# Optimization experiments

Measured on AMD Instinct MI355X. Metric: run time of the kernel, lower is better.

## Reference

```python
import jax, jax.numpy as jnp
import numpy as np

N = 20000      # nodes
E = 320000     # edges
F = 32         # node_feat_dim
H = 128        # hidden_dim
HEADS = 4
DH = 128       # out_channels per head (PyG TransformerConv semantics)
L = 2          # number of GNNBlocks actually built


def _ln(x, s, b, eps=1e-5):
    m = x.mean(-1, keepdims=True)
    v = ((x - m) ** 2).mean(-1, keepdims=True)
    return (x - m) / jnp.sqrt(v + eps) * s + b


def setup_inputs() -> dict:
    key = jax.random.key(0)
    ks = jax.random.split(key, 16)
    nrm = lambda k, sh, sc=0.05: jax.random.normal(k, sh, dtype=jnp.float32) * sc
    inp = {}
    inp['x'] = jax.random.normal(ks[0], (N, F), dtype=jnp.float32)
    inp['edge_index'] = jax.random.randint(ks[1], (2, E), 0, N)
    inp['Win'] = nrm(ks[2], (F, H))
    inp['b_in'] = jnp.zeros((H,), jnp.float32)
    inp['ln1_s'] = jnp.ones((L, H), jnp.float32)
    inp['ln1_b'] = jnp.zeros((L, H), jnp.float32)
    inp['Wq'] = nrm(ks[3], (L, H, HEADS * DH))
    inp['bq'] = jnp.zeros((L, HEADS * DH), jnp.float32)
    inp['Wk'] = nrm(ks[4], (L, H, HEADS * DH))
    inp['bk'] = jnp.zeros((L, HEADS * DH), jnp.float32)
    inp['Wv'] = nrm(ks[5], (L, H, HEADS * DH))
    inp['bv'] = jnp.zeros((L, HEADS * DH), jnp.float32)
    inp['Wskip'] = nrm(ks[6], (L, H, H))
    inp['bskip'] = jnp.zeros((L, H), jnp.float32)
    inp['Wbeta'] = nrm(ks[7], (L, 3 * H, 1))
    inp['ln2_s'] = jnp.ones((L, H), jnp.float32)
    inp['ln2_b'] = jnp.zeros((L, H), jnp.float32)
    inp['W1'] = nrm(ks[8], (L, H, 4 * H))
    inp['b1'] = jnp.zeros((L, 4 * H), jnp.float32)
    inp['W2'] = nrm(ks[9], (L, 4 * H, H))
    inp['b2'] = jnp.zeros((L, H), jnp.float32)
    inp['g1'] = jnp.ones((L,), jnp.float32)
    inp['g2'] = jnp.ones((L,), jnp.float32)
    inp['lno_s'] = jnp.ones((H,), jnp.float32)
    inp['lno_b'] = jnp.zeros((H,), jnp.float32)
    return inp


def reference(x, edge_index, Win, b_in, ln1_s, ln1_b, Wq, bq, Wk, bk, Wv, bv,
              Wskip, bskip, Wbeta, ln2_s, ln2_b, W1, b1, W2, b2, g1, g2,
              lno_s, lno_b):
    src, dst = edge_index[0], edge_index[1]  # messages flow src -> dst
    n = x.shape[0]
    scale = 1.0 / np.sqrt(DH).astype(np.float32)
    h = x @ Win + b_in  # [N,H]
    for l in range(L):
        # --- pre-norm TransformerConv (heads=4, concat=False, beta=True) ---
        hn = _ln(h, ln1_s[l], ln1_b[l])
        q = (hn @ Wq[l] + bq[l]).reshape(n, HEADS, DH)
        k = (hn @ Wk[l] + bk[l]).reshape(n, HEADS, DH)
        v = (hn @ Wv[l] + bv[l]).reshape(n, HEADS, DH)
        # per-edge attention logits [E, HEADS]
        alpha = jnp.einsum('ehd,ehd->eh', q[dst], k[src]) * scale
        # segment softmax over incoming edges of each target node
        amax = jax.ops.segment_max(alpha, dst, num_segments=n)  # [N,HEADS]
        num = jnp.exp(alpha - amax[dst])
        den = jax.ops.segment_sum(num, dst, num_segments=n)      # [N,HEADS]
        a = num / den[dst]                                       # [E,HEADS]
        # scatter-aggregate weighted values, then mean over heads (concat=False)
        agg = jax.ops.segment_sum(a[:, :, None] * v[src], dst, num_segments=n)
        out = agg.mean(axis=1)                                   # [N,H]
        # root skip + beta gate
        xr = hn @ Wskip[l] + bskip[l]
        beta = jax.nn.sigmoid(
            jnp.concatenate([out, xr, out - xr], axis=-1) @ Wbeta[l])  # [N,1]
        attn = beta * xr + (1.0 - beta) * out
        h = h + g1[l] * attn
        # --- pre-norm FFN ---
        hn2 = _ln(h, ln2_s[l], ln2_b[l])
        ffn = jax.nn.gelu(hn2 @ W1[l] + b1[l], approximate=False) @ W2[l] + b2[l]
        h = h + g2[l] * ffn
    return _ln(h, lno_s, lno_b)
```

## Files before the change

### kernel.cpp

```cpp
#include <hip/hip_runtime.h>
#include <hip/hip_bf16.h>
#include <math.h>

#define NN 20000
#define NE 320000

typedef unsigned short ushort_t;
typedef unsigned short ushortx8 __attribute__((ext_vector_type(8)));
typedef short s16x8 __attribute__((ext_vector_type(8)));
typedef float f32x4 __attribute__((ext_vector_type(4)));
typedef float f32x2 __attribute__((ext_vector_type(2)));

__device__ __forceinline__ float us2f(unsigned short u){
  return __uint_as_float(((unsigned)u) << 16);
}
__device__ __forceinline__ unsigned short f2us(float f){
  unsigned u = __float_as_uint(f);
  unsigned r = (u + 0x7fffu + ((u >> 16) & 1u)) >> 16;
  return (unsigned short)r;
}
__device__ __forceinline__ void e4m3x8_to_f32(uint2 d, float* out){
  f32x2 a = __builtin_amdgcn_cvt_pk_f32_fp8(d.x, false);
  f32x2 b = __builtin_amdgcn_cvt_pk_f32_fp8(d.x, true);
  f32x2 c = __builtin_amdgcn_cvt_pk_f32_fp8(d.y, false);
  f32x2 e = __builtin_amdgcn_cvt_pk_f32_fp8(d.y, true);
  out[0] = a.x; out[1] = a.y; out[2] = b.x; out[3] = b.y;
  out[4] = c.x; out[5] = c.y; out[6] = e.x; out[7] = e.y;
}
__device__ __forceinline__ uint2 f32x8_to_e4m3(const float* f){
  unsigned lo = __builtin_amdgcn_cvt_pk_fp8_f32(f[0], f[1], 0u, false);
  lo = __builtin_amdgcn_cvt_pk_fp8_f32(f[2], f[3], lo, true);
  unsigned hi = __builtin_amdgcn_cvt_pk_fp8_f32(f[4], f[5], 0u, false);
  hi = __builtin_amdgcn_cvt_pk_fp8_f32(f[6], f[7], hi, true);
  return make_uint2(lo, hi);
}

__global__ void k_hist(const int* __restrict__ ei, int* __restrict__ deg){
  int e = blockIdx.x * 256 + threadIdx.x;
  if (e < NE) atomicAdd(&deg[ei[NE + e]], 1);
}

__global__ __launch_bounds__(1024) void k_scan(const int* __restrict__ deg,
                                               int* __restrict__ rowst,
                                               int* __restrict__ cur){
  __shared__ int s[1024];
  __shared__ int carry_s;
  int tid = threadIdx.x;
  if (tid == 0) carry_s = 0;
  __syncthreads();
  for (int base = 0; base < NN; base += 1024){
    int v = (base + tid < NN) ? deg[base + tid] : 0;
    s[tid] = v; __syncthreads();
    for (int off = 1; off < 1024; off <<= 1){
      int t = (tid >= off) ? s[tid - off] : 0;
      __syncthreads();
      s[tid] += t;
      __syncthreads();
    }
    int carry = carry_s;
    int excl = carry + s[tid] - v;
    if (base + tid < NN){ rowst[base + tid] = excl; cur[base + tid] = excl; }
    __syncthreads();
    if (tid == 0) carry_s = carry + s[1023];
    __syncthreads();
  }
  if (tid == 0) rowst[NN] = carry_s;
}

__global__ void k_scatter(const int* __restrict__ ei, int* __restrict__ cur,
                          int* __restrict__ srcs){
  int e = blockIdx.x * 256 + threadIdx.x;
  if (e < NE){
    int s = ei[e];
    int d = ei[NE + e];
    int p = atomicAdd(&cur[d], 1);
    srcs[p] = s;
  }
}

__global__ void k_wt(const float* __restrict__ Wq, const float* __restrict__ Wk,
                     const float* __restrict__ Wv, const float* __restrict__ Wsk,
                     const float* __restrict__ W1, const float* __restrict__ W2,
                     const float* __restrict__ bq, const float* __restrict__ bk,
                     const float* __restrict__ bv, const float* __restrict__ bsk,
                     ushort_t* __restrict__ out, float* __restrict__ bcat,
                     int* __restrict__ deg){
  int f = blockIdx.x * 256 + threadIdx.x;
  if (f < 688128){
    float val;
    if (f < 425984){
      int l = f / 212992, idx = f % 212992;
      int n = idx / 128, kk = idx % 128;
      if (n < 512)       val = Wq[(size_t)l * 65536 + kk * 512 + n];
      else if (n < 1024) val = Wk[(size_t)l * 65536 + kk * 512 + (n - 512)];
      else if (n < 1536) val = Wv[(size_t)l * 65536 + kk * 512 + (n - 1024)];
      else               val = Wsk[(size_t)l * 16384 + kk * 128 + (n - 1536)];
    } else if (f < 557056){
      int idx = f - 425984;
      int l = idx / 65536, r = idx % 65536;
      int n = r / 128, kk = r % 128;
      val = W1[(size_t)l * 65536 + kk * 512 + n];
    } else {
      int idx = f - 557056;
      int l = idx / 65536, r = idx % 65536;
      int n = r / 512, kk = r % 512;
      val = W2[(size_t)l * 65536 + kk * 128 + n];
    }
    out[f] = f2us(val);
  } else if (f < 691456){
    int i = f - 688128;
    int l = i / 1664, c = i % 1664;
    float v;
    if (c < 512)       v = bq[l * 512 + c];
    else if (c < 1024) v = bk[l * 512 + c - 512];
    else if (c < 1536) v = bv[l * 512 + c - 1024];
    else               v = bsk[l * 128 + c - 1536];
    bcat[i] = v;
  } else if (f < 711456){
    deg[f - 691456] = 0;
  }
}

__global__ __launch_bounds__(128) void k_inproj(const float* __restrict__ x,
                                                const float* __restrict__ Win,
                                                const float* __restrict__ bin,
                                                float* __restrict__ h){
  __shared__ float sW[32 * 128];
  __shared__ float sx[4][32];
  int tid = threadIdx.x;
  for (int i = 0; i < 32; i++) sW[i * 128 + tid] = Win[i * 128 + tid];
  int r0 = blockIdx.x * 4;
  {
    int r = tid >> 5, kk = tid & 31;
    int gr = r0 + r;
    sx[r][kk] = (gr < NN) ? x[gr * 32 + kk] : 0.f;
  }
  __syncthreads();
  float bias = bin[tid];
  for (int r = 0; r < 4; r++){
    int gr = r0 + r;
    if (gr >= NN) break;
    float acc = bias;
    #pragma unroll
    for (int k2 = 0; k2 < 32; k2++) acc += sx[r][k2] * sW[k2 * 128 + tid];
    h[(size_t)gr * 128 + tid] = acc;
  }
}

template<int OUTBF16>
__global__ void k_ln(const float* __restrict__ in, const float* __restrict__ sc,
                     const float* __restrict__ bi, void* __restrict__ outp, int rows){
  int row = blockIdx.x * 4 + (threadIdx.x >> 6);
  int lane = threadIdx.x & 63;
  if (row >= rows) return;
  const float* p = in + (size_t)row * 128 + lane * 2;
  float x0 = p[0], x1 = p[1];
  float sum = x0 + x1;
  for (int m = 1; m < 64; m <<= 1) sum += __shfl_xor(sum, m);
  float mean = sum * (1.f / 128.f);
  float d0 = x0 - mean, d1 = x1 - mean;
  float vs = d0 * d0 + d1 * d1;
  for (int m = 1; m < 64; m <<= 1) vs += __shfl_xor(vs, m);
  float rstd = rsqrtf(vs * (1.f / 128.f) + 1e-5f);
  int d = lane * 2;
  float o0 = d0 * rstd * sc[d] + bi[d];
  float o1 = d1 * rstd * sc[d + 1] + bi[d + 1];
  if (OUTBF16){
    ushort_t* o = (ushort_t*)outp + (size_t)row * 128 + d;
    o[0] = f2us(o0); o[1] = f2us(o1);
  } else {
    float* o = (float*)outp + (size_t)row * 128 + d;
    o[0] = o0; o[1] = o1;
  }
}

template<int MODE>
__global__ __launch_bounds__(256) void k_mm(const ushort_t* __restrict__ A, int M, int K,
                                            const ushort_t* __restrict__ Bt,
                                            const float* __restrict__ bias,
                                            void* __restrict__ Cp, int ldc,
                                            const float* __restrict__ gptr,
                                            ushort_t* __restrict__ qout,
                                            unsigned char* __restrict__ kvout,
                                            ushort_t* __restrict__ xrout){
  __shared__ ushort_t smem[2 * 128 * 72];
  ushort_t* As = smem;
  ushort_t* Bs = smem + 128 * 72;
  int tid = threadIdx.x;
  int m0 = blockIdx.x * 128, n0 = blockIdx.y * 128;
  int lane = tid & 63, w = tid >> 6;
  int wm = (w >> 1) * 64, wn = (w & 1) * 64;
  int fr = lane & 15, fq = lane >> 4;
  f32x4 acc[4][4];
  #pragma unroll
  for (int i = 0; i < 4; i++)
    #pragma unroll
    for (int j = 0; j < 4; j++) acc[i][j] = (f32x4){0.f, 0.f, 0.f, 0.f};

  for (int k0 = 0; k0 < K; k0 += 64){
    __syncthreads();
    #pragma unroll
    for (int it = 0; it < 4; it++){
      int idx = it * 256 + tid;
      int row = idx >> 3, ks = (idx & 7) * 8;
      int gr = m0 + row; if (gr >= M) gr = M - 1;
      *(ushortx8*)&As[row * 72 + ks] = *(const ushortx8*)(A + (size_t)gr * K + k0 + ks);
      *(ushortx8*)&Bs[row * 72 + ks] = *(const ushortx8*)(Bt + (size_t)(n0 + row) * K + k0 + ks);
    }
    __syncthreads();
    #pragma unroll
    for (int ks = 0; ks < 64; ks += 32){
      s16x8 a[4], b[4];
      #pragma unroll
      for (int i = 0; i < 4; i++)
        a[i] = *(const s16x8*)&As[(wm + i * 16 + fr) * 72 + ks + fq * 8];
      #pragma unroll
      for (int j = 0; j < 4; j++)
        b[j] = *(const s16x8*)&Bs[(wn + j * 16 + fr) * 72 + ks + fq * 8];
      #pragma unroll
      for (int i = 0; i < 4; i++)
        #pragma unroll
        for (int j = 0; j < 4; j++)
          acc[i][j] = __builtin_amdgcn_mfma_f32_16x16x32_bf16(a[i], b[j], acc[i][j], 0, 0, 0);
    }
  }

  if (MODE == 2){
    float g = *gptr;
    #pragma unroll
    for (int i = 0; i < 4; i++){
      int grb = m0 + wm + i * 16 + fq * 4;
      #pragma unroll
      for (int r = 0; r < 4; r++){
        int gr = grb + r;
        if (gr >= M) continue;
        #pragma unroll
        for (int j = 0; j < 4; j++){
          int gc = n0 + wn + j * 16 + fr;
          float c = acc[i][j][r] + bias[gc];
          ((float*)Cp)[(size_t)gr * ldc + gc] += g * c;
        }
      }
    }
    return;
  }

  __syncthreads();
  ushort_t* Cs = smem;
  #pragma unroll
  for (int i = 0; i < 4; i++){
    int rowb = wm + i * 16 + fq * 4;
    #pragma unroll
    for (int j = 0; j < 4; j++){
      int col = wn + j * 16 + fr;
      float bv = bias[n0 + col];
      #pragma unroll
      for (int r = 0; r < 4; r++){
        float c = acc[i][j][r] + bv;
        if (MODE == 1) c = 0.5f * c * (1.f + erff(c * 0.70710678118654752f));
        Cs[(rowb + r) * 136 + col] = f2us(c);
      }
    }
  }
  __syncthreads();
  #pragma unroll
  for (int it = 0; it < 8; it++){
    int idx = it * 256 + tid;
    int row = idx >> 4, seg = idx & 15;
    int gr = m0 + row;
    if (gr >= M) continue;
    ushortx8 cv = *(const ushortx8*)&Cs[row * 136 + seg * 8];
    int gc = n0 + seg * 8;
    if (MODE == 1){
      *(ushortx8*)((ushort_t*)Cp + (size_t)gr * ldc + gc) = cv;
    } else {
      if (n0 < 512){
        *(ushortx8*)(qout + (size_t)gr * 512 + gc) = cv;
      } else if (n0 < 1536){
        float fv[8];
        #pragma unroll
        for (int t = 0; t < 8; t++) fv[t] = us2f(cv[t]);
        *(uint2*)(kvout + (size_t)gr * 1024 + (gc - 512)) = f32x8_to_e4m3(fv);
      } else {
        *(ushortx8*)(xrout + (size_t)gr * 128 + (gc - 1536)) = cv;
      }
    }
  }
}

__global__ void k_alpha(const ushort_t* __restrict__ q, const unsigned char* __restrict__ kv8,
                        const int* __restrict__ rowst, const int* __restrict__ srcs,
                        float* __restrict__ alw){
  int n = blockIdx.x * 4 + (threadIdx.x >> 6);
  int lane = threadIdx.x & 63;
  if (n >= NN) return;
  int s0 = rowst[n], s1 = rowst[n + 1];
  if (s0 == s1) return;
  ushortx8 qv = *((const ushortx8*)(q + (size_t)n * 512) + lane);
  float qf[8];
  #pragma unroll
  for (int t = 0; t < 8; t++) qf[t] = us2f(qv[t]);
  const float scale = 0.08838834764831845f;
  int head = lane >> 4;
  for (int c0 = s0; c0 < s1; c0 += 64){
    int rem = s1 - c0; if (rem > 64) rem = 64;
    int se = (lane < rem) ? srcs[c0 + lane] : 0;
    int j = 0;
    for (; j + 4 <= rem; j += 4){
      int sv[4];
      #pragma unroll
      for (int u = 0; u < 4; u++) sv[u] = __shfl(se, j + u);
      uint2 kd[4];
      #pragma unroll
      for (int u = 0; u < 4; u++)
        kd[u] = *((const uint2*)(kv8 + (size_t)sv[u] * 1024) + lane);
      float p[4] = {0.f, 0.f, 0.f, 0.f};
      #pragma unroll
      for (int u = 0; u < 4; u++){
        float kf[8];
        e4m3x8_to_f32(kd[u], kf);
        #pragma unroll
        for (int t = 0; t < 8; t++) p[u] += qf[t] * kf[t];
      }
      #pragma unroll
      for (int u = 0; u < 4; u++){
        p[u] += __shfl_xor(p[u], 1); p[u] += __shfl_xor(p[u], 2);
        p[u] += __shfl_xor(p[u], 4); p[u] += __shfl_xor(p[u], 8);
      }
      if ((lane & 15) == 0){
        #pragma unroll
        for (int u = 0; u < 4; u++) alw[(size_t)(c0 + j + u) * 4 + head] = __expf(p[u] * scale);
      }
    }
    for (; j < rem; j++){
      int sv0 = __shfl(se, j);
      uint2 kd = *((const uint2*)(kv8 + (size_t)sv0 * 1024) + lane);
      float kf[8];
      e4m3x8_to_f32(kd, kf);
      float p0 = 0.f;
      #pragma unroll
      for (int t = 0; t < 8; t++) p0 += qf[t] * kf[t];
      p0 += __shfl_xor(p0, 1); p0 += __shfl_xor(p0, 2);
      p0 += __shfl_xor(p0, 4); p0 += __shfl_xor(p0, 8);
      if ((lane & 15) == 0) alw[(size_t)(c0 + j) * 4 + head] = __expf(p0 * scale);
    }
  }
}

__global__ void k_node(const float* __restrict__ alw, const unsigned char* __restrict__ kv8,
                       const int* __restrict__ rowst, const int* __restrict__ srcs,
                       const ushort_t* __restrict__ xr, const float* __restrict__ Wb,
                       const float* __restrict__ g1p, float* __restrict__ h,
                       const float* __restrict__ sc2, const float* __restrict__ bi2,
                       ushort_t* __restrict__ hn){
  int n = blockIdx.x * 4 + (threadIdx.x >> 6);
  int lane = threadIdx.x & 63;
  if (n >= NN) return;
  int s0 = rowst[n], s1 = rowst[n + 1];
  int deg = s1 - s0;
  int head = lane >> 4;
  float l = 0.f;
  float acc[8] = {0.f, 0.f, 0.f, 0.f, 0.f, 0.f, 0.f, 0.f};
  for (int c0 = s0; c0 < s1; c0 += 64){
    int rem = s1 - c0; if (rem > 64) rem = 64;
    int se = (lane < rem) ? srcs[c0 + lane] : 0;
    int j = 0;
    for (; j + 4 <= rem; j += 4){
      int sv[4];
      #pragma unroll
      for (int u = 0; u < 4; u++) sv[u] = __shfl(se, j + u);
      uint2 vd[4];
      #pragma unroll
      for (int u = 0; u < 4; u++)
        vd[u] = *((const uint2*)(kv8 + (size_t)sv[u] * 1024 + 512) + lane);
      float wv[4];
      #pragma unroll
      for (int u = 0; u < 4; u++) wv[u] = alw[(size_t)(c0 + j + u) * 4 + head];
      #pragma unroll
      for (int u = 0; u < 4; u++){
        float vf[8];
        e4m3x8_to_f32(vd[u], vf);
        l += wv[u];
        #pragma unroll
        for (int t = 0; t < 8; t++) acc[t] += wv[u] * vf[t];
      }
    }
    for (; j < rem; j++){
      int sv0 = __shfl(se, j);
      uint2 vd = *((const uint2*)(kv8 + (size_t)sv0 * 1024 + 512) + lane);
      float vf[8];
      e4m3x8_to_f32(vd, vf);
      float ww = alw[(size_t)(c0 + j) * 4 + head];
      l += ww;
      #pragma unroll
      for (int t = 0; t < 8; t++) acc[t] += ww * vf[t];
    }
  }
  float inv = deg ? (0.25f / l) : 0.f;
  #pragma unroll
  for (int t = 0; t < 8; t++){
    float r = acc[t] * inv;
    r += __shfl_xor(r, 16); r += __shfl_xor(r, 32);
    acc[t] = r;
  }
  if (lane < 16){
    int d = lane * 8;
    float xv[8];
    {
      ushortx8 xrv = *(const ushortx8*)(xr + (size_t)n * 128 + d);
      #pragma unroll
      for (int t = 0; t < 8; t++) xv[t] = us2f(xrv[t]);
    }
    float pp = 0.f;
    #pragma unroll
    for (int t = 0; t < 8; t++){
      float w0 = Wb[d + t], w1 = Wb[128 + d + t], w2 = Wb[256 + d + t];
      pp += acc[t] * (w0 + w2) + xv[t] * (w1 - w2);
    }
    pp += __shfl_xor(pp, 1); pp += __shfl_xor(pp, 2);
    pp += __shfl_xor(pp, 4); pp += __shfl_xor(pp, 8);
    float beta = 1.f / (1.f + __expf(-pp));
    float g = *g1p;
    float* hp = h + (size_t)n * 128 + d;
    float hv[8];
    {
      float4 h0 = *(const float4*)(hp);
      float4 h1 = *(const float4*)(hp + 4);
      hv[0]=h0.x; hv[1]=h0.y; hv[2]=h0.z; hv[3]=h0.w;
      hv[4]=h1.x; hv[5]=h1.y; hv[6]=h1.z; hv[7]=h1.w;
    }
    #pragma unroll
    for (int t = 0; t < 8; t++)
      hv[t] += g * (beta * xv[t] + (1.f - beta) * acc[t]);
    float s = 0.f;
    #pragma unroll
    for (int t = 0; t < 8; t++) s += hv[t];
    s += __shfl_xor(s, 1); s += __shfl_xor(s, 2);
    s += __shfl_xor(s, 4); s += __shfl_xor(s, 8);
    float mean = s * (1.f / 128.f);
    float vs = 0.f;
    #pragma unroll
    for (int t = 0; t < 8; t++){ float dd = hv[t] - mean; vs += dd * dd; }
    vs += __shfl_xor(vs, 1); vs += __shfl_xor(vs, 2);
    vs += __shfl_xor(vs, 4); vs += __shfl_xor(vs, 8);
    float rstd = rsqrtf(vs * (1.f / 128.f) + 1e-5f);
    *(float4*)(hp) = make_float4(hv[0], hv[1], hv[2], hv[3]);
    *(float4*)(hp + 4) = make_float4(hv[4], hv[5], hv[6], hv[7]);
    ushortx8 hno;
    #pragma unroll
    for (int t = 0; t < 8; t++)
      hno[t] = f2us((hv[t] - mean) * rstd * sc2[d + t] + bi2[d + t]);
    *(ushortx8*)(hn + (size_t)n * 128 + d) = hno;
  }
}

extern "C" void kernel_launch(void* const* d_in, const int* in_sizes, int n_in,
                              void* d_out, int out_size, void* d_ws, size_t ws_size,
                              hipStream_t stream){
  const float* x    = (const float*)d_in[0];
  const int*   ei   = (const int*)d_in[1];
  const float* Win  = (const float*)d_in[2];
  const float* bin  = (const float*)d_in[3];
  const float* ln1s = (const float*)d_in[4];
  const float* ln1b = (const float*)d_in[5];
  const float* Wq   = (const float*)d_in[6];
  const float* bq   = (const float*)d_in[7];
  const float* Wk   = (const float*)d_in[8];
  const float* bk   = (const float*)d_in[9];
  const float* Wv   = (const float*)d_in[10];
  const float* bv   = (const float*)d_in[11];
  const float* Wsk  = (const float*)d_in[12];
  const float* bsk  = (const float*)d_in[13];
  const float* Wbt  = (const float*)d_in[14];
  const float* ln2s = (const float*)d_in[15];
  const float* ln2b = (const float*)d_in[16];
  const float* W1   = (const float*)d_in[17];
  const float* b1   = (const float*)d_in[18];
  const float* W2   = (const float*)d_in[19];
  const float* b2   = (const float*)d_in[20];
  const float* g1   = (const float*)d_in[21];
  const float* g2   = (const float*)d_in[22];
  const float* lnos = (const float*)d_in[23];
  const float* lnob = (const float*)d_in[24];

  char* wsb = (char*)d_ws;
  size_t off = 0;
  float*         h    = (float*)(wsb + off);         off += (size_t)NN * 128 * 4;
  ushort_t*      hn   = (ushort_t*)(wsb + off);      off += (size_t)NN * 128 * 2;
  ushort_t*      qbuf = (ushort_t*)(wsb + off);      off += (size_t)NN * 512 * 2;
  unsigned char* kv8  = (unsigned char*)(wsb + off); off += (size_t)NN * 1024;
  ushort_t*      xrb  = (ushort_t*)(wsb + off);      off += (size_t)NN * 128 * 2;
  ushort_t*      tb   = (ushort_t*)(wsb + off);      off += (size_t)NN * 512 * 2;
  float*         alw  = (float*)(wsb + off);         off += (size_t)NE * 4 * 4;
  ushort_t*      wt   = (ushort_t*)(wsb + off);      off += (size_t)688128 * 2;
  float*         bcat = (float*)(wsb + off);         off += (size_t)3328 * 4;
  int*           deg   = (int*)(wsb + off);          off += (size_t)NN * 4;
  int*           rowst = (int*)(wsb + off);          off += (size_t)(NN + 4) * 4;
  int*           cur   = (int*)(wsb + off);          off += (size_t)NN * 4;
  int*           srcs  = (int*)(wsb + off);          off += (size_t)NE * 4;
  ushort_t* Wcat = wt;
  ushort_t* W1t  = wt + 425984;
  ushort_t* W2t  = wt + 557056;

  k_wt<<<2780, 256, 0, stream>>>(Wq, Wk, Wv, Wsk, W1, W2, bq, bk, bv, bsk, wt, bcat, deg);
  k_hist<<<(NE + 255) / 256, 256, 0, stream>>>(ei, deg);
  k_scan<<<1, 1024, 0, stream>>>(deg, rowst, cur);
  k_scatter<<<(NE + 255) / 256, 256, 0, stream>>>(ei, cur, srcs);
  k_inproj<<<(NN + 3) / 4, 128, 0, stream>>>(x, Win, bin, h);

  dim3 gQ(157, 13), gF1(157, 4), gF2(157, 1);
  for (int l = 0; l < 2; l++){
    k_ln<1><<<(NN + 3) / 4, 256, 0, stream>>>(h, ln1s + l * 128, ln1b + l * 128, hn, NN);
    k_mm<3><<<gQ, 256, 0, stream>>>(hn, NN, 128, Wcat + (size_t)l * 212992, bcat + l * 1664,
                                    nullptr, 0, nullptr, qbuf, kv8, xrb);
    k_alpha<<<(NN + 3) / 4, 256, 0, stream>>>(qbuf, kv8, rowst, srcs, alw);
    k_node<<<(NN + 3) / 4, 256, 0, stream>>>(alw, kv8, rowst, srcs, xrb, Wbt + l * 384,
                                             g1 + l, h, ln2s + l * 128, ln2b + l * 128, hn);
    k_mm<1><<<gF1, 256, 0, stream>>>(hn, NN, 128, W1t + (size_t)l * 65536, b1 + l * 512,
                                     tb, 512, nullptr, nullptr, nullptr, nullptr);
    k_mm<2><<<gF2, 256, 0, stream>>>(tb, NN, 512, W2t + (size_t)l * 65536, b2 + l * 128,
                                     h, 128, g2 + l, nullptr, nullptr, nullptr);
  }
  k_ln<0><<<(NN + 3) / 4, 256, 0, stream>>>(h, lnos, lnob, (float*)d_out, NN);
}
```

Before: 465.1 us.

## Fuse attention logits into aggregation with interleaved fp8 K/V layout

Merges the separate logit kernel into the node aggregation kernel, so exp(q·k) weights are computed on the fly and the per-edge weight buffer is no longer written and reread. K and V fp8 rows are interleaved per 8-element chunk so one 16-byte load per lane fetches both K and V for an edge. It also replaces the shared-memory scan with a wave-shuffle scan and makes the input projection process 16 rows per block. The cost is more work and registers per thread in the fused kernel, which may reduce occupancy.

```diff
diff --git a/kernel.cpp b/kernel.cpp
--- a/kernel.cpp
+++ b/kernel.cpp
@@ -43,28 +43,34 @@
 __global__ __launch_bounds__(1024) void k_scan(const int* __restrict__ deg,
                                                int* __restrict__ rowst,
                                                int* __restrict__ cur){
-  __shared__ int s[1024];
-  __shared__ int carry_s;
+  __shared__ int ws[16];
   int tid = threadIdx.x;
-  if (tid == 0) carry_s = 0;
-  __syncthreads();
+  int lane = tid & 63, wid = tid >> 6;
+  int carry = 0;
   for (int base = 0; base < NN; base += 1024){
-    int v = (base + tid < NN) ? deg[base + tid] : 0;
-    s[tid] = v; __syncthreads();
-    for (int off = 1; off < 1024; off <<= 1){
-      int t = (tid >= off) ? s[tid - off] : 0;
-      __syncthreads();
-      s[tid] += t;
-      __syncthreads();
-    }
-    int carry = carry_s;
-    int excl = carry + s[tid] - v;
-    if (base + tid < NN){ rowst[base + tid] = excl; cur[base + tid] = excl; }
+    int i = base + tid;
+    int v = (i < NN) ? deg[i] : 0;
+    int incl = v;
+    #pragma unroll
+    for (int off = 1; off < 64; off <<= 1){
+      int t = __shfl_up(incl, off);
+      if (lane >= off) incl += t;
+    }
+    if (lane == 63) ws[wid] = incl;
     __syncthreads();
-    if (tid == 0) carry_s = carry + s[1023];
+    int tot = 0, woff = 0;
+    #pragma unroll
+    for (int k2 = 0; k2 < 16; k2++){
+      int wv = ws[k2];
+      tot += wv;
+      if (k2 < wid) woff += wv;
+    }
+    int excl = carry + woff + incl - v;
+    if (i < NN){ rowst[i] = excl; cur[i] = excl; }
+    carry += tot;
     __syncthreads();
   }
-  if (tid == 0) rowst[NN] = carry_s;
+  if (tid == 0) rowst[NN] = carry;
 }
 
 __global__ void k_scatter(const int* __restrict__ ei, int* __restrict__ cur,
@@ -126,18 +132,17 @@
                                                 const float* __restrict__ bin,
                                                 float* __restrict__ h){
   __shared__ float sW[32 * 128];
-  __shared__ float sx[4][32];
+  __shared__ float sx[16][32];
   int tid = threadIdx.x;
   for (int i = 0; i < 32; i++) sW[i * 128 + tid] = Win[i * 128 + tid];
-  int r0 = blockIdx.x * 4;
-  {
-    int r = tid >> 5, kk = tid & 31;
-    int gr = r0 + r;
-    sx[r][kk] = (gr < NN) ? x[gr * 32 + kk] : 0.f;
+  int r0 = blockIdx.x * 16;
+  for (int rr = tid >> 5; rr < 16; rr += 4){
+    int gr = r0 + rr;
+    sx[rr][tid & 31] = (gr < NN) ? x[(size_t)gr * 32 + (tid & 31)] : 0.f;
   }
   __syncthreads();
   float bias = bin[tid];
-  for (int r = 0; r < 4; r++){
+  for (int r = 0; r < 16; r++){
     int gr = r0 + r;
     if (gr >= NN) break;
     float acc = bias;
@@ -280,7 +285,12 @@
         float fv[8];
         #pragma unroll
         for (int t = 0; t < 8; t++) fv[t] = us2f(cv[t]);
-        *(uint2*)(kvout + (size_t)gr * 1024 + (gc - 512)) = f32x8_to_e4m3(fv);
+        uint2 pk = f32x8_to_e4m3(fv);
+        if (n0 < 1024){
+          *(uint2*)(kvout + (size_t)gr * 1024 + (size_t)((gc - 512) >> 3) * 16) = pk;
+        } else {
+          *(uint2*)(kvout + (size_t)gr * 1024 + (size_t)((gc - 1024) >> 3) * 16 + 8) = pk;
+        }
       } else {
         *(ushortx8*)(xrout + (size_t)gr * 128 + (gc - 1536)) = cv;
       }
@@ -288,66 +298,7 @@
   }
 }
 
-__global__ void k_alpha(const ushort_t* __restrict__ q, const unsigned char* __restrict__ kv8,
-                        const int* __restrict__ rowst, const int* __restrict__ srcs,
-                        float* __restrict__ alw){
-  int n = blockIdx.x * 4 + (threadIdx.x >> 6);
-  int lane = threadIdx.x & 63;
-  if (n >= NN) return;
-  int s0 = rowst[n], s1 = rowst[n + 1];
-  if (s0 == s1) return;
-  ushortx8 qv = *((const ushortx8*)(q + (size_t)n * 512) + lane);
-  float qf[8];
-  #pragma unroll
-  for (int t = 0; t < 8; t++) qf[t] = us2f(qv[t]);
-  const float scale = 0.08838834764831845f;
-  int head = lane >> 4;
-  for (int c0 = s0; c0 < s1; c0 += 64){
-    int rem = s1 - c0; if (rem > 64) rem = 64;
-    int se = (lane < rem) ? srcs[c0 + lane] : 0;
-    int j = 0;
-    for (; j + 4 <= rem; j += 4){
-      int sv[4];
-      #pragma unroll
-      for (int u = 0; u < 4; u++) sv[u] = __shfl(se, j + u);
-      uint2 kd[4];
-      #pragma unroll
-      for (int u = 0; u < 4; u++)
-        kd[u] = *((const uint2*)(kv8 + (size_t)sv[u] * 1024) + lane);
-      float p[4] = {0.f, 0.f, 0.f, 0.f};
-      #pragma unroll
-      for (int u = 0; u < 4; u++){
-        float kf[8];
-        e4m3x8_to_f32(kd[u], kf);
-        #pragma unroll
-        for (int t = 0; t < 8; t++) p[u] += qf[t] * kf[t];
-      }
-      #pragma unroll
-      for (int u = 0; u < 4; u++){
-        p[u] += __shfl_xor(p[u], 1); p[u] += __shfl_xor(p[u], 2);
-        p[u] += __shfl_xor(p[u], 4); p[u] += __shfl_xor(p[u], 8);
-      }
-      if ((lane & 15) == 0){
-        #pragma unroll
-        for (int u = 0; u < 4; u++) alw[(size_t)(c0 + j + u) * 4 + head] = __expf(p[u] * scale);
-      }
-    }
-    for (; j < rem; j++){
-      int sv0 = __shfl(se, j);
-      uint2 kd = *((const uint2*)(kv8 + (size_t)sv0 * 1024) + lane);
-      float kf[8];
-      e4m3x8_to_f32(kd, kf);
-      float p0 = 0.f;
-      #pragma unroll
-      for (int t = 0; t < 8; t++) p0 += qf[t] * kf[t];
-      p0 += __shfl_xor(p0, 1); p0 += __shfl_xor(p0, 2);
-      p0 += __shfl_xor(p0, 4); p0 += __shfl_xor(p0, 8);
-      if ((lane & 15) == 0) alw[(size_t)(c0 + j) * 4 + head] = __expf(p0 * scale);
-    }
-  }
-}
-
-__global__ void k_node(const float* __restrict__ alw, const unsigned char* __restrict__ kv8,
+__global__ void k_attn(const ushort_t* __restrict__ q, const unsigned char* __restrict__ kv8,
                        const int* __restrict__ rowst, const int* __restrict__ srcs,
                        const ushort_t* __restrict__ xr, const float* __restrict__ Wb,
                        const float* __restrict__ g1p, float* __restrict__ h,
@@ -358,7 +309,13 @@
   if (n >= NN) return;
   int s0 = rowst[n], s1 = rowst[n + 1];
   int deg = s1 - s0;
-  int head = lane >> 4;
+  float qf[8];
+  {
+    ushortx8 qv = *((const ushortx8*)(q + (size_t)n * 512) + lane);
+    #pragma unroll
+    for (int t = 0; t < 8; t++) qf[t] = us2f(qv[t]);
+  }
+  const float scale = 0.08838834764831845f;
   float l = 0.f;
   float acc[8] = {0.f, 0.f, 0.f, 0.f, 0.f, 0.f, 0.f, 0.f};
   for (int c0 = s0; c0 < s1; c0 += 64){
@@ -369,31 +326,49 @@
       int sv[4];
       #pragma unroll
       for (int u = 0; u < 4; u++) sv[u] = __shfl(se, j + u);
-      uint2 vd[4];
+      uint4 kvd[4];
       #pragma unroll
       for (int u = 0; u < 4; u++)
-        vd[u] = *((const uint2*)(kv8 + (size_t)sv[u] * 1024 + 512) + lane);
-      float wv[4];
-      #pragma unroll
-      for (int u = 0; u < 4; u++) wv[u] = alw[(size_t)(c0 + j + u) * 4 + head];
+        kvd[u] = *((const uint4*)(kv8 + (size_t)sv[u] * 1024) + lane);
+      float p[4] = {0.f, 0.f, 0.f, 0.f};
       #pragma unroll
       for (int u = 0; u < 4; u++){
+        float kf[8];
+        e4m3x8_to_f32(make_uint2(kvd[u].x, kvd[u].y), kf);
+        #pragma unroll
+        for (int t = 0; t < 8; t++) p[u] += qf[t] * kf[t];
+      }
+      #pragma unroll
+      for (int u = 0; u < 4; u++){
+        p[u] += __shfl_xor(p[u], 1); p[u] += __shfl_xor(p[u], 2);
+        p[u] += __shfl_xor(p[u], 4); p[u] += __shfl_xor(p[u], 8);
+      }
+      #pragma unroll
+      for (int u = 0; u < 4; u++){
+        float w = __expf(p[u] * scale);
         float vf[8];
-        e4m3x8_to_f32(vd[u], vf);
-        l += wv[u];
+        e4m3x8_to_f32(make_uint2(kvd[u].z, kvd[u].w), vf);
+        l += w;
         #pragma unroll
-        for (int t = 0; t < 8; t++) acc[t] += wv[u] * vf[t];
+        for (int t = 0; t < 8; t++) acc[t] += w * vf[t];
       }
     }
     for (; j < rem; j++){
       int sv0 = __shfl(se, j);
-      uint2 vd = *((const uint2*)(kv8 + (size_t)sv0 * 1024 + 512) + lane);
+      uint4 kvd = *((const uint4*)(kv8 + (size_t)sv0 * 1024) + lane);
+      float kf[8];
+      e4m3x8_to_f32(make_uint2(kvd.x, kvd.y), kf);
+      float p0 = 0.f;
+      #pragma unroll
+      for (int t = 0; t < 8; t++) p0 += qf[t] * kf[t];
+      p0 += __shfl_xor(p0, 1); p0 += __shfl_xor(p0, 2);
+      p0 += __shfl_xor(p0, 4); p0 += __shfl_xor(p0, 8);
+      float w = __expf(p0 * scale);
       float vf[8];
-      e4m3x8_to_f32(vd, vf);
-      float ww = alw[(size_t)(c0 + j) * 4 + head];
-      l += ww;
-      #pragma unroll
-      for (int t = 0; t < 8; t++) acc[t] += ww * vf[t];
+      e4m3x8_to_f32(make_uint2(kvd.z, kvd.w), vf);
+      l += w;
+      #pragma unroll
+      for (int t = 0; t < 8; t++) acc[t] += w * vf[t];
     }
   }
   float inv = deg ? (0.25f / l) : 0.f;
@@ -491,7 +466,6 @@
   unsigned char* kv8  = (unsigned char*)(wsb + off); off += (size_t)NN * 1024;
   ushort_t*      xrb  = (ushort_t*)(wsb + off);      off += (size_t)NN * 128 * 2;
   ushort_t*      tb   = (ushort_t*)(wsb + off);      off += (size_t)NN * 512 * 2;
-  float*         alw  = (float*)(wsb + off);         off += (size_t)NE * 4 * 4;
   ushort_t*      wt   = (ushort_t*)(wsb + off);      off += (size_t)688128 * 2;
   float*         bcat = (float*)(wsb + off);         off += (size_t)3328 * 4;
   int*           deg   = (int*)(wsb + off);          off += (size_t)NN * 4;
@@ -506,15 +480,14 @@
   k_hist<<<(NE + 255) / 256, 256, 0, stream>>>(ei, deg);
   k_scan<<<1, 1024, 0, stream>>>(deg, rowst, cur);
   k_scatter<<<(NE + 255) / 256, 256, 0, stream>>>(ei, cur, srcs);
-  k_inproj<<<(NN + 3) / 4, 128, 0, stream>>>(x, Win, bin, h);
+  k_inproj<<<(NN + 15) / 16, 128, 0, stream>>>(x, Win, bin, h);
 
   dim3 gQ(157, 13), gF1(157, 4), gF2(157, 1);
   for (int l = 0; l < 2; l++){
     k_ln<1><<<(NN + 3) / 4, 256, 0, stream>>>(h, ln1s + l * 128, ln1b + l * 128, hn, NN);
     k_mm<3><<<gQ, 256, 0, stream>>>(hn, NN, 128, Wcat + (size_t)l * 212992, bcat + l * 1664,
                                     nullptr, 0, nullptr, qbuf, kv8, xrb);
-    k_alpha<<<(NN + 3) / 4, 256, 0, stream>>>(qbuf, kv8, rowst, srcs, alw);
-    k_node<<<(NN + 3) / 4, 256, 0, stream>>>(alw, kv8, rowst, srcs, xrb, Wbt + l * 384,
+    k_attn<<<(NN + 3) / 4, 256, 0, stream>>>(qbuf, kv8, rowst, srcs, xrb, Wbt + l * 384,
                                              g1 + l, h, ln2s + l * 128, ln2b + l * 128, hn);
     k_mm<1><<<gF1, 256, 0, stream>>>(hn, NN, 128, W1t + (size_t)l * 65536, b1 + l * 512,
                                      tb, 512, nullptr, nullptr, nullptr, nullptr);
```

Result: faster. 443.3 us (-4.7%).
